# Kernel optimization log

Measured on AMD Instinct MI355X. Metric: run time of the kernel, lower is better.

## Reference

```python
import jax, jax.numpy as jnp
import numpy as np

VOCAB, E, H, B, T = 32000, 256, 512, 64, 512
PAD = VOCAB - 1


def setup_inputs() -> dict:
    key = jax.random.key(0)
    ks = jax.random.split(key, 9)
    s_ih = 1.0 / np.sqrt(H)
    inp = {
        "x": jax.random.randint(ks[0], (B, T), 0, VOCAB, dtype=jnp.int64 if jax.config.jax_enable_x64 else jnp.int32),
        "length": jax.random.randint(ks[1], (B, 1), 1, T + 1, dtype=jnp.int32),
        "embed_table": (jax.random.normal(ks[2], (VOCAB, E), dtype=jnp.float32)).at[PAD].set(0.0),
        "W_ih": jax.random.uniform(ks[3], (4 * H, E), jnp.float32, -s_ih, s_ih),
        "W_hh": jax.random.uniform(ks[4], (4 * H, H), jnp.float32, -s_ih, s_ih),
        "b_ih": jax.random.uniform(ks[5], (4 * H,), jnp.float32, -s_ih, s_ih),
        "b_hh": jax.random.uniform(ks[6], (4 * H,), jnp.float32, -s_ih, s_ih),
        "W_cls": jax.random.uniform(ks[7], (2, H), jnp.float32, -s_ih, s_ih),
        "b_cls": jax.random.uniform(ks[8], (2,), jnp.float32, -s_ih, s_ih),
    }
    return inp


def _lstm(xg, W_hh):
    # xg: [T, B, 4H] precomputed input-side gate activations; PyTorch gate order i,f,g,o
    Bn = xg.shape[1]
    h0 = jnp.zeros((Bn, H), xg.dtype)
    c0 = jnp.zeros((Bn, H), xg.dtype)

    def step(carry, g_in):
        h, c = carry
        g = g_in + h @ W_hh.T
        i, f, gg, o = jnp.split(g, 4, axis=-1)
        c = jax.nn.sigmoid(f) * c + jax.nn.sigmoid(i) * jnp.tanh(gg)
        h = jax.nn.sigmoid(o) * jnp.tanh(c)
        return (h, c), h

    _, hs = jax.lax.scan(step, (h0, c0), xg)
    return hs  # [T, B, H]


def reference(x, length, embed_table, W_ih, W_hh, b_ih, b_hh, W_cls, b_cls):
    emb_tab = embed_table.at[PAD].set(0.0)  # padding_idx row is zero
    we = emb_tab[x]  # [B, T, E]
    xg = jnp.einsum("bte,ge->btg", we, W_ih) + b_ih + b_hh  # [B, T, 4H]
    hs = _lstm(jnp.swapaxes(xg, 0, 1), W_hh)  # [T, B, H]
    hs = jnp.swapaxes(hs, 0, 1)  # [B, T, H]
    # ragged max-pool over valid timesteps
    mask = jnp.arange(T)[None, :] < length  # [B, T]
    neg = jnp.finfo(hs.dtype).min
    feature = jnp.max(jnp.where(mask[:, :, None], hs, neg), axis=1)  # [B, H]
    return feature @ W_cls.T + b_cls
```

## Files before the change

### kernel.cpp

```cpp
#include <hip/hip_runtime.h>
#include <hip/hip_bf16.h>

#define EN 256
#define HN 512
#define BN 64
#define TN 512
#define NBLK 64
#define KCAT 1280
#define NBUF 8
#define SLOTB 65536

typedef __attribute__((ext_vector_type(8))) short short8;
typedef __attribute__((ext_vector_type(4))) short short4v;
typedef __attribute__((ext_vector_type(4))) float f32x4;

#define SCOPE __HIP_MEMORY_SCOPE_AGENT
#define MFMA(A, B, C) __builtin_amdgcn_mfma_f32_16x16x32_bf16((A), (B), (C), 0, 0, 0)

__device__ inline short bf_of(float f) {
  __hip_bfloat16 h = __float2bfloat16(f);
  return *reinterpret_cast<short*>(&h);
}
__device__ inline float f_of_bf(short s) {
  __hip_bfloat16 h = *reinterpret_cast<__hip_bfloat16*>(&s);
  return __bfloat162float(h);
}

__global__ __launch_bounds__(256) void zero_kernel(unsigned* hb_u32,
                                                   unsigned* flags) {
  int idx = blockIdx.x * 256 + threadIdx.x;
  if (idx < SLOTB / 4)
    __hip_atomic_store(&hb_u32[idx], 0u, __ATOMIC_RELAXED, SCOPE);
  if (idx < NBLK)
    __hip_atomic_store(&flags[idx], 0u, __ATOMIC_RELAXED, SCOPE);
}

__global__ __launch_bounds__(256) void gather_kernel(
    short* __restrict__ weB, const int* __restrict__ x,
    const float* __restrict__ emb) {
  const int t = blockIdx.x;
  const int tid = threadIdx.x;
  const int b = tid >> 2, q = tid & 3;
  const int row = x[b * TN + t];
  const float4* src = (const float4*)(emb + (size_t)row * EN + q * 64);
  short* dst = weB + ((size_t)(t * 64 + b)) * EN + q * 64;
#pragma unroll
  for (int i = 0; i < 16; i++) {
    float4 v = src[i];
    short4v o = { bf_of(v.x), bf_of(v.y), bf_of(v.z), bf_of(v.w) };
    *(short4v*)(dst + i * 4) = o;
  }
}

__global__ __launch_bounds__(256) void prep_w_kernel(
    short* __restrict__ Wall, const float* __restrict__ Wih,
    const float* __restrict__ Whh) {
  int idx = blockIdx.x * 256 + threadIdx.x;
  int grow = idx / KCAT, kc = idx - grow * KCAT;
  float v;
  if (kc < 256) {
    v = Wih[(size_t)grow * EN + kc];
  } else if (kc < 768) {
    v = Whh[(size_t)grow * HN + (kc - 256)];
  } else {
    float f = Whh[(size_t)grow * HN + (kc - 768)];
    v = f - f_of_bf(bf_of(f));
  }
  Wall[idx] = bf_of(v);
}

__device__ __forceinline__ void poll_flags(const unsigned* flags,
                                           unsigned want, int l) {
  bool done = false;
  while (true) {
    if (!done) {
      unsigned v = __hip_atomic_load(&flags[l], __ATOMIC_RELAXED, SCOPE);
      done = (v >= want);
    }
    if (__all(done ? 1 : 0)) break;
    __builtin_amdgcn_s_sleep(2);
  }
  asm volatile("" ::: "memory");
}

#define HLOAD16                                                             \
  asm volatile(                                                             \
    "global_load_dwordx4 %0,  %16, off sc1\n\t"                             \
    "global_load_dwordx4 %1,  %16, off offset:1024 sc1\n\t"                 \
    "global_load_dwordx4 %2,  %16, off offset:2048 sc1\n\t"                 \
    "global_load_dwordx4 %3,  %16, off offset:3072 sc1\n\t"                 \
    "global_load_dwordx4 %4,  %17, off sc1\n\t"                             \
    "global_load_dwordx4 %5,  %17, off offset:1024 sc1\n\t"                 \
    "global_load_dwordx4 %6,  %17, off offset:2048 sc1\n\t"                 \
    "global_load_dwordx4 %7,  %17, off offset:3072 sc1\n\t"                 \
    "global_load_dwordx4 %8,  %18, off sc1\n\t"                             \
    "global_load_dwordx4 %9,  %18, off offset:1024 sc1\n\t"                 \
    "global_load_dwordx4 %10, %18, off offset:2048 sc1\n\t"                 \
    "global_load_dwordx4 %11, %18, off offset:3072 sc1\n\t"                 \
    "global_load_dwordx4 %12, %19, off sc1\n\t"                             \
    "global_load_dwordx4 %13, %19, off offset:1024 sc1\n\t"                 \
    "global_load_dwordx4 %14, %19, off offset:2048 sc1\n\t"                 \
    "global_load_dwordx4 %15, %19, off offset:3072 sc1\n\t"                 \
    "s_waitcnt vmcnt(0)"                                                    \
    : "=&v"(hv0), "=&v"(hv1), "=&v"(hv2),  "=&v"(hv3),                      \
      "=&v"(hv4), "=&v"(hv5), "=&v"(hv6),  "=&v"(hv7),                      \
      "=&v"(hv8), "=&v"(hv9), "=&v"(hv10), "=&v"(hv11),                     \
      "=&v"(hv12), "=&v"(hv13), "=&v"(hv14), "=&v"(hv15)                    \
    : "v"(hb0), "v"(hb1), "v"(hb2), "v"(hb3) : "memory")

__global__ __launch_bounds__(512, 1) void scan_kernel(
    const short* __restrict__ weB, const short* __restrict__ Wall,
    char* __restrict__ hb, const int* __restrict__ length,
    const float* __restrict__ bih, const float* __restrict__ bhh,
    const float* __restrict__ Wcls, const float* __restrict__ bcls,
    float* __restrict__ part, unsigned* flags, float* __restrict__ out) {
  __shared__ float gl[32][65];
  __shared__ __align__(16) short hstage[BN][8];
  const int tid = threadIdx.x;
  const int l = tid & 63, w = tid >> 6;
  const int bid = blockIdx.x;
  const int j0 = bid * 8;

  const int btile = (w & 3) * 16;
  const int rhalf = (w >> 2) * 16;

  short8 aH[24], aL[16];
  {
    int r = rhalf + (l & 15);
    int grow = (r >> 3) * HN + j0 + (r & 7);
    const short* wp = Wall + (size_t)grow * KCAT + 8 * (l >> 4);
#pragma unroll
    for (int kk = 0; kk < 24; kk++) aH[kk] = *(const short8*)(wp + kk * 32);
#pragma unroll
    for (int kk = 0; kk < 16; kk++) aL[kk] = *(const short8*)(wp + 768 + kk * 32);
  }

  const int jj = w, b = l;
  float bias[4];
#pragma unroll
  for (int ty = 0; ty < 4; ty++) {
    int grow = ty * HN + j0 + jj;
    bias[ty] = bih[grow] + bhh[grow];
  }
  const int len = length[b];
  float c = 0.f, fmx = -INFINITY;

  const int cons_off = (l >> 4) * 16384 + (btile + (l & 15)) * 16;
  const int prod_off = (bid & 3) * 16384 + (bid >> 2) * 1024 + l * 16;

  for (int t = 0; t < TN; t++) {
    const short* xrow = weB + ((size_t)(t * 64 + btile + (l & 15))) * EN + 8 * (l >> 4);
    short8 xf[8];
#pragma unroll
    for (int kk = 0; kk < 8; kk++) xf[kk] = *(const short8*)(xrow + kk * 32);
    f32x4 accH = {0.f, 0.f, 0.f, 0.f}, accL = {0.f, 0.f, 0.f, 0.f};
#pragma unroll
    for (int kk = 0; kk < 8; kk++)
      accH = MFMA(aH[kk], xf[kk], accH);

    if (w == 0) poll_flags(flags, (unsigned)t, l);
    __syncthreads();

    const char* hb0 = hb + (size_t)(t & 7) * SLOTB + cons_off;
    const char* hb1 = hb0 + 4096;
    const char* hb2 = hb0 + 8192;
    const char* hb3 = hb0 + 12288;
    short8 hv0, hv1, hv2, hv3, hv4, hv5, hv6, hv7;
    short8 hv8, hv9, hv10, hv11, hv12, hv13, hv14, hv15;
    HLOAD16;
    accH = MFMA(aH[8],  hv0,  accH);  accL = MFMA(aL[0],  hv0,  accL);
    accH = MFMA(aH[9],  hv1,  accH);  accL = MFMA(aL[1],  hv1,  accL);
    accH = MFMA(aH[10], hv2,  accH);  accL = MFMA(aL[2],  hv2,  accL);
    accH = MFMA(aH[11], hv3,  accH);  accL = MFMA(aL[3],  hv3,  accL);
    accH = MFMA(aH[12], hv4,  accH);  accL = MFMA(aL[4],  hv4,  accL);
    accH = MFMA(aH[13], hv5,  accH);  accL = MFMA(aL[5],  hv5,  accL);
    accH = MFMA(aH[14], hv6,  accH);  accL = MFMA(aL[6],  hv6,  accL);
    accH = MFMA(aH[15], hv7,  accH);  accL = MFMA(aL[7],  hv7,  accL);
    accH = MFMA(aH[16], hv8,  accH);  accL = MFMA(aL[8],  hv8,  accL);
    accH = MFMA(aH[17], hv9,  accH);  accL = MFMA(aL[9],  hv9,  accL);
    accH = MFMA(aH[18], hv10, accH);  accL = MFMA(aL[10], hv10, accL);
    accH = MFMA(aH[19], hv11, accH);  accL = MFMA(aL[11], hv11, accL);
    accH = MFMA(aH[20], hv12, accH);  accL = MFMA(aL[12], hv12, accL);
    accH = MFMA(aH[21], hv13, accH);  accL = MFMA(aL[13], hv13, accL);
    accH = MFMA(aH[22], hv14, accH);  accL = MFMA(aL[14], hv14, accL);
    accH = MFMA(aH[23], hv15, accH);  accL = MFMA(aL[15], hv15, accL);

#pragma unroll
    for (int q = 0; q < 4; q++) {
      int r = rhalf + (l >> 4) * 4 + q;
      gl[r][btile + (l & 15)] = accH[q] + accL[q];
    }
    __syncthreads();
    {
      float gi = gl[0 + jj][b] + bias[0];
      float gf = gl[8 + jj][b] + bias[1];
      float gg = gl[16 + jj][b] + bias[2];
      float go = gl[24 + jj][b] + bias[3];
      float si = 1.f / (1.f + __expf(-gi));
      float sf = 1.f / (1.f + __expf(-gf));
      float so = 1.f / (1.f + __expf(-go));
      float tg = 2.f / (1.f + __expf(-2.f * gg)) - 1.f;
      c = sf * c + si * tg;
      float tc = 2.f / (1.f + __expf(-2.f * c)) - 1.f;
      float h = so * tc;
      hstage[b][jj] = bf_of(h);
      if (t < len) fmx = fmaxf(fmx, h);
    }
    __syncthreads();
    if (w == 0) {
      short8 val = *(const short8*)&hstage[l][0];
      char* dp = hb + (size_t)((t + 1) & 7) * SLOTB + prod_off;
      asm volatile("global_store_dwordx4 %0, %1, off sc1"
                   :: "v"(dp), "v"(val) : "memory");
      asm volatile("s_waitcnt vmcnt(0)" ::: "memory");
      if (l == 0)
        __hip_atomic_store(&flags[bid], (unsigned)(t + 1),
                           __ATOMIC_RELAXED, SCOPE);
    }
  }

  gl[jj][b]      = fmx * Wcls[j0 + jj];
  gl[8 + jj][b]  = fmx * Wcls[HN + j0 + jj];
  __syncthreads();
  if (tid < 128) {
    int cls = tid >> 6, bb = tid & 63;
    float s = 0.f;
#pragma unroll
    for (int q = 0; q < 8; q++) s += gl[cls * 8 + q][bb];
    __hip_atomic_store(&part[(size_t)bid * 128 + cls * 64 + bb], s,
                       __ATOMIC_RELAXED, SCOPE);
  }
  __syncthreads();
  asm volatile("s_waitcnt vmcnt(0)" ::: "memory");
  if (tid == 0)
    __hip_atomic_store(&flags[bid], (unsigned)(TN + 1), __ATOMIC_RELAXED, SCOPE);
  if (bid == 0) {
    if (w == 0) poll_flags(flags, (unsigned)(TN + 1), l);
    __syncthreads();
    if (tid < 128) {
      int cls = tid >> 6, bb = tid & 63;
      float s = bcls[cls];
#pragma unroll 8
      for (int k = 0; k < NBLK; k++)
        s += __uint_as_float(__hip_atomic_load(
            (const unsigned*)&part[(size_t)k * 128 + cls * 64 + bb],
            __ATOMIC_RELAXED, SCOPE));
      out[bb * 2 + cls] = s;
    }
  }
}

extern "C" void kernel_launch(void* const* d_in, const int* in_sizes, int n_in,
                              void* d_out, int out_size, void* d_ws, size_t ws_size,
                              hipStream_t stream) {
  const int*   x    = (const int*)d_in[0];
  const int*   len  = (const int*)d_in[1];
  const float* emb  = (const float*)d_in[2];
  const float* Wih  = (const float*)d_in[3];
  const float* Whh  = (const float*)d_in[4];
  const float* bih  = (const float*)d_in[5];
  const float* bhh  = (const float*)d_in[6];
  const float* Wcls = (const float*)d_in[7];
  const float* bcls = (const float*)d_in[8];
  float* out = (float*)d_out;

  char* ws = (char*)d_ws;
  short* weB  = (short*)ws;
  short* Wall = (short*)(ws + 16777216ull);
  char*  hb   = ws + 16777216ull + 5242880;
  float* part = (float*)(ws + 16777216ull + 5242880 + 524288);
  unsigned* flagp = (unsigned*)(ws + 16777216ull + 5242880 + 524288 + 32768);

  zero_kernel<<<dim3(64), dim3(256), 0, stream>>>((unsigned*)hb, flagp);
  gather_kernel<<<dim3(TN), dim3(256), 0, stream>>>(weB, x, emb);
  prep_w_kernel<<<dim3((2048 * KCAT) / 256), dim3(256), 0, stream>>>(Wall, Wih, Whh);

  void* args[] = { (void*)&weB, (void*)&Wall, (void*)&hb, (void*)&len,
                   (void*)&bih, (void*)&bhh, (void*)&Wcls, (void*)&bcls,
                   (void*)&part, (void*)&flagp, (void*)&out };
  hipLaunchCooperativeKernel((void*)scan_kernel, dim3(NBLK), dim3(512),
                             args, 0, stream);
}
```

Measured before the change: 2.348 ms.

## Replace per-step flag polling with NaN-sentinel data-validity polling on hidden-state buffers

Removes the per-timestep flag barrier: producers no longer wait for their store to complete and then publish a flag, and consumers no longer poll flags followed by a block-wide syncthreads. Instead each wave spins on the hidden-state ring buffer itself until no loaded vector holds a NaN sentinel value. After consuming a slot, the block re-poisons the slot it last consumed so it can be reused. The intent is to take the flag round-trip and the block barrier off the recurrent critical path. In exchange every wave now polls global memory, and correctness relies on 16-byte stores becoming visible as a unit and on the sentinel pattern never appearing as a real bf16 h value.

```diff
diff --git a/kernel.cpp b/kernel.cpp
--- a/kernel.cpp
+++ b/kernel.cpp
@@ -9,10 +9,12 @@
 #define KCAT 1280
 #define NBUF 8
 #define SLOTB 65536
+#define SENTU 0x7FC07FC0u
 
 typedef __attribute__((ext_vector_type(8))) short short8;
 typedef __attribute__((ext_vector_type(4))) short short4v;
 typedef __attribute__((ext_vector_type(4))) float f32x4;
+typedef __attribute__((ext_vector_type(4))) int int4v;
 
 #define SCOPE __HIP_MEMORY_SCOPE_AGENT
 #define MFMA(A, B, C) __builtin_amdgcn_mfma_f32_16x16x32_bf16((A), (B), (C), 0, 0, 0)
@@ -28,9 +30,12 @@
 
 __global__ __launch_bounds__(256) void zero_kernel(unsigned* hb_u32,
                                                    unsigned* flags) {
+  const int total = NBUF * SLOTB / 4;
+  for (int i = blockIdx.x * 256 + threadIdx.x; i < total; i += 64 * 256) {
+    unsigned v = (i < SLOTB / 4) ? 0u : SENTU;
+    __hip_atomic_store(&hb_u32[i], v, __ATOMIC_RELAXED, SCOPE);
+  }
   int idx = blockIdx.x * 256 + threadIdx.x;
-  if (idx < SLOTB / 4)
-    __hip_atomic_store(&hb_u32[idx], 0u, __ATOMIC_RELAXED, SCOPE);
   if (idx < NBLK)
     __hip_atomic_store(&flags[idx], 0u, __ATOMIC_RELAXED, SCOPE);
 }
@@ -108,6 +113,9 @@
       "=&v"(hv12), "=&v"(hv13), "=&v"(hv14), "=&v"(hv15)                    \
     : "v"(hb0), "v"(hb1), "v"(hb2), "v"(hb3) : "memory")
 
+#define CHK(v) ((((const int4v&)(v)).x != (int)SENTU) &                     \
+                (((const int4v&)(v)).w != (int)SENTU))
+
 __global__ __launch_bounds__(512, 1) void scan_kernel(
     const short* __restrict__ weB, const short* __restrict__ Wall,
     char* __restrict__ hb, const int* __restrict__ length,
@@ -145,6 +153,10 @@
   const int len = length[b];
   float c = 0.f, fmx = -INFINITY;
 
+  short8 sentv;
+#pragma unroll
+  for (int i = 0; i < 8; i++) sentv[i] = (short)0x7FC0;
+
   const int cons_off = (l >> 4) * 16384 + (btile + (l & 15)) * 16;
   const int prod_off = (bid & 3) * 16384 + (bid >> 2) * 1024 + l * 16;
 
@@ -157,9 +169,6 @@
 #pragma unroll
     for (int kk = 0; kk < 8; kk++)
       accH = MFMA(aH[kk], xf[kk], accH);
-
-    if (w == 0) poll_flags(flags, (unsigned)t, l);
-    __syncthreads();
 
     const char* hb0 = hb + (size_t)(t & 7) * SLOTB + cons_off;
     const char* hb1 = hb0 + 4096;
@@ -167,7 +176,22 @@
     const char* hb3 = hb0 + 12288;
     short8 hv0, hv1, hv2, hv3, hv4, hv5, hv6, hv7;
     short8 hv8, hv9, hv10, hv11, hv12, hv13, hv14, hv15;
-    HLOAD16;
+    while (true) {
+      HLOAD16;
+      int ok = CHK(hv0)  & CHK(hv1)  & CHK(hv2)  & CHK(hv3)
+             & CHK(hv4)  & CHK(hv5)  & CHK(hv6)  & CHK(hv7)
+             & CHK(hv8)  & CHK(hv9)  & CHK(hv10) & CHK(hv11)
+             & CHK(hv12) & CHK(hv13) & CHK(hv14) & CHK(hv15);
+      if (__all(ok)) break;
+      __builtin_amdgcn_s_sleep(1);
+    }
+
+    if (w == 1) {
+      char* rp = hb + (size_t)((t + 7) & 7) * SLOTB + prod_off;
+      asm volatile("global_store_dwordx4 %0, %1, off sc1"
+                   :: "v"(rp), "v"(sentv) : "memory");
+    }
+
     accH = MFMA(aH[8],  hv0,  accH);  accL = MFMA(aL[0],  hv0,  accL);
     accH = MFMA(aH[9],  hv1,  accH);  accL = MFMA(aL[1],  hv1,  accL);
     accH = MFMA(aH[10], hv2,  accH);  accL = MFMA(aL[2],  hv2,  accL);
@@ -212,10 +236,6 @@
       char* dp = hb + (size_t)((t + 1) & 7) * SLOTB + prod_off;
       asm volatile("global_store_dwordx4 %0, %1, off sc1"
                    :: "v"(dp), "v"(val) : "memory");
-      asm volatile("s_waitcnt vmcnt(0)" ::: "memory");
-      if (l == 0)
-        __hip_atomic_store(&flags[bid], (unsigned)(t + 1),
-                           __ATOMIC_RELAXED, SCOPE);
     }
   }
 
@@ -233,9 +253,9 @@
   __syncthreads();
   asm volatile("s_waitcnt vmcnt(0)" ::: "memory");
   if (tid == 0)
-    __hip_atomic_store(&flags[bid], (unsigned)(TN + 1), __ATOMIC_RELAXED, SCOPE);
+    __hip_atomic_store(&flags[bid], 1u, __ATOMIC_RELAXED, SCOPE);
   if (bid == 0) {
-    if (w == 0) poll_flags(flags, (unsigned)(TN + 1), l);
+    if (w == 0) poll_flags(flags, 1u, l);
     __syncthreads();
     if (tid < 128) {
       int cls = tid >> 6, bb = tid & 63;
```

Result: slower. 3.168 ms (+34.9%).
